# Performance work log

Hardware: AMD Instinct MI355X
Metric: run time of the kernel (lower is better)

The kernel has to match this reference:

```python
import jax, jax.numpy as jnp
import numpy as np

N_HEAD = 16


def setup_inputs() -> dict:
    key = jax.random.key(0)
    k1, k2, k3 = jax.random.split(key, 3)
    B, T, C = 2, 2048, 1024
    x = jax.random.normal(k1, (B, T, C), dtype=jnp.float32)
    Wqkv = jax.random.normal(k2, (C, 3 * C), dtype=jnp.float32) * 0.02
    bqkv = jnp.zeros((3 * C,), dtype=jnp.float32)
    Wproj = jax.random.normal(k3, (C, C), dtype=jnp.float32) * 0.02
    bproj = jnp.zeros((C,), dtype=jnp.float32)
    return {"x": x, "Wqkv": Wqkv, "bqkv": bqkv, "Wproj": Wproj, "bproj": bproj}


def reference(x, Wqkv, bqkv, Wproj, bproj):
    b, t, c = x.shape
    h = N_HEAD
    d = c // h  # head_dim
    # qkv projection, split into q,k,v per head: (b,t,3,h,d)
    qkv = (x @ Wqkv + bqkv).reshape(b, t, 3, h, d)
    q, k, v = qkv[:, :, 0], qkv[:, :, 1], qkv[:, :, 2]  # each (b,t,h,d)
    # Faithful quirk of original: n_state = head_dim // heads, scale = 1/sqrt(n_state)
    scale = jnp.float32(1.0 / np.sqrt(d // h))
    # attn_mode == 'all': dense non-causal attention
    w = jnp.einsum('bqhd,bkhd->bhqk', q, k)  # (b,h,t,t)
    w = jax.nn.softmax(w * scale, axis=-1)
    a = jnp.einsum('bhqk,bkhd->bqhd', w, v).reshape(b, t, c)
    return a @ Wproj + bproj
```

## Files before the change

### kernel.cpp

```cpp
#include <hip/hip_runtime.h>

typedef float floatx4 __attribute__((ext_vector_type(4)));
typedef float floatx16 __attribute__((ext_vector_type(16)));
typedef __bf16 bf16x8 __attribute__((ext_vector_type(8)));
typedef __bf16 bf16x4 __attribute__((ext_vector_type(4)));
typedef __bf16 bf16x2 __attribute__((ext_vector_type(2)));
typedef float floatx2 __attribute__((ext_vector_type(2)));

#define MFMA16 __builtin_amdgcn_mfma_f32_16x16x32_bf16
#define MFMA32 __builtin_amdgcn_mfma_f32_32x32x16_bf16

typedef const __attribute__((address_space(1))) void* gas_t;
typedef __attribute__((address_space(3))) void* las_t;
#define GLD16(g, l) __builtin_amdgcn_global_load_lds((gas_t)(g), (las_t)(l), 16, 0, 0)

static __device__ __forceinline__ unsigned short f2bf(float f) {
  union { float f; unsigned int u; } v; v.f = f;
  unsigned int r = v.u + 0x7fffu + ((v.u >> 16) & 1u);
  return (unsigned short)(r >> 16);
}

static __device__ __forceinline__ unsigned pk2(float a, float b) {
  floatx2 v; v[0] = a; v[1] = b;
  union { bf16x2 h; unsigned u; } u;
  u.h = __builtin_convertvector(v, bf16x2);
  return u.u;
}

static __device__ __forceinline__ void cast_transpose_tile(
    const float* __restrict__ in, unsigned short* __restrict__ out,
    int R, int C, int bx, int by) {
  const int r0 = by * 64, c0 = bx * 64;
  const int tid = threadIdx.x;
  __shared__ float tl[64][65];
  const int rr = tid >> 4, cc = (tid & 15) * 4;
#pragma unroll
  for (int i = 0; i < 4; ++i) {
    int row = rr + i * 16;
    float4 v = *(const float4*)(in + (size_t)(r0 + row) * C + c0 + cc);
    tl[row][cc] = v.x; tl[row][cc + 1] = v.y;
    tl[row][cc + 2] = v.z; tl[row][cc + 3] = v.w;
  }
  __syncthreads();
  const int cl = tid >> 2, rbase = (tid & 3) * 16;
  unsigned short o[16];
#pragma unroll
  for (int j = 0; j < 16; ++j) o[j] = f2bf(tl[rbase + j][cl]);
  unsigned short* dst = out + (size_t)(c0 + cl) * R + r0 + rbase;
  *(uint4*)dst = *(uint4*)o;
  *(uint4*)(dst + 8) = *(uint4*)(o + 8);
}

__global__ __launch_bounds__(256) void prologue_kernel(
    const float* __restrict__ x, unsigned short* __restrict__ Xb,
    const float* __restrict__ Wqkv, unsigned short* __restrict__ Wqkvt,
    const float* __restrict__ Wproj, unsigned short* __restrict__ Wprojt) {
  const int bid = blockIdx.x;
  if (bid < 4096) {
    int i = bid * 256 + threadIdx.x;
    float4 v = ((const float4*)x)[i];
    ushort4 o;
    o.x = f2bf(v.x); o.y = f2bf(v.y); o.z = f2bf(v.z); o.w = f2bf(v.w);
    ((ushort4*)Xb)[i] = o;
  } else if (bid < 4096 + 768) {
    int b2 = bid - 4096;
    cast_transpose_tile(Wqkv, Wqkvt, 1024, 3072, b2 % 48, b2 / 48);
  } else {
    int b3 = bid - 4096 - 768;
    cast_transpose_tile(Wproj, Wprojt, 1024, 1024, b3 % 16, b3 / 16);
  }
}

__global__ __launch_bounds__(256) void gemm_qkv(
    const unsigned short* __restrict__ A,
    const unsigned short* __restrict__ Bt,
    const float* __restrict__ bias,
    unsigned short* __restrict__ Q,
    unsigned short* __restrict__ Kc,
    unsigned short* __restrict__ Vt) {
  const int K = 1024;
  const int m0 = blockIdx.y * 128, n0 = blockIdx.x * 128;
  const int tid = threadIdx.x, w = tid >> 6, l = tid & 63;
  const int l16 = l & 15, lq = l >> 4;
  const int wm = w >> 1, wn = w & 1;
  const int which = n0 >> 10;

  __shared__ __align__(16) unsigned short SH[16384];
  unsigned short* As = SH;
  unsigned short* Bs = SH + 8192;

  floatx4 acc[4][4] = {};

  int sA[4], sB[4];
  unsigned ldso[4];
#pragma unroll
  for (int j = 0; j < 4; ++j) {
    int s = j * 256 + tid;
    int row = s >> 3, blk = (s & 7) ^ (row & 7);
    sA[j] = (m0 + row) * K + blk * 8;
    sB[j] = (n0 + row) * K + blk * 8;
    ldso[j] = (unsigned)(j * 256 + w * 64) * 8;
  }

  if (which == 2) {
    for (int k0 = 0; k0 < K; k0 += 64) {
      __syncthreads();
#pragma unroll
      for (int j = 0; j < 4; ++j) {
        GLD16(A + sA[j] + k0, As + ldso[j]);
        GLD16(Bt + sB[j] + k0, Bs + ldso[j]);
      }
      __syncthreads();
#pragma unroll
      for (int kk = 0; kk < 2; ++kk) {
        bf16x8 af[4], bf[4];
#pragma unroll
        for (int mi = 0; mi < 4; ++mi) {
          int row = wm * 64 + mi * 16 + l16;
          int blk = (kk * 4 + lq) ^ (l16 & 7);
          af[mi] = *(const bf16x8*)(As + row * 64 + blk * 8);
        }
#pragma unroll
        for (int ni = 0; ni < 4; ++ni) {
          int row = wn * 64 + ni * 16 + l16;
          int blk = (kk * 4 + lq) ^ (l16 & 7);
          bf[ni] = *(const bf16x8*)(Bs + row * 64 + blk * 8);
        }
#pragma unroll
        for (int ni = 0; ni < 4; ++ni)
#pragma unroll
          for (int mi = 0; mi < 4; ++mi)
            acc[mi][ni] = MFMA16(af[mi], bf[ni], acc[mi][ni], 0, 0, 0);
      }
    }
    float bv[4];
#pragma unroll
    for (int ni = 0; ni < 4; ++ni) bv[ni] = bias[n0 + wn * 64 + ni * 16 + l16];
    __syncthreads();
    unsigned short* E = SH + w * 2304;
    const int bh = (m0 >> 11) * 16 + ((n0 & 1023) >> 6) + wn;
    const int tt0 = (m0 & 2047) + wm * 64;
    const int m8 = l & 7, bc = 16 * (m8 >> 1) + 4 * (m8 & 1);
#pragma unroll
    for (int p = 0; p < 2; ++p) {
#pragma unroll
      for (int n2 = 0; n2 < 2; ++n2) {
        int ni = p * 2 + n2;
#pragma unroll
        for (int mi = 0; mi < 4; ++mi) {
          floatx4 vv = acc[mi][ni] + bv[ni];
          *(bf16x4*)(E + (n2 * 16 + l16) * 72 + mi * 16 + lq * 4) =
              __builtin_convertvector(vv, bf16x4);
        }
      }
#pragma unroll
      for (int s = 0; s < 4; ++s) {
        int dl = s * 8 + (l >> 3);
        union { bf16x4 h[2]; bf16x8 v; } uu;
        uu.h[0] = *(const bf16x4*)(E + dl * 72 + bc);
        uu.h[1] = *(const bf16x4*)(E + dl * 72 + bc + 8);
        *(bf16x8*)(Vt + ((size_t)bh * 64 + p * 32 + dl) * 2048 + tt0 +
                   m8 * 8) = uu.v;
      }
    }
  } else {
    for (int k0 = 0; k0 < K; k0 += 64) {
      __syncthreads();
#pragma unroll
      for (int j = 0; j < 4; ++j) {
        GLD16(A + sA[j] + k0, As + ldso[j]);
        GLD16(Bt + sB[j] + k0, Bs + ldso[j]);
      }
      __syncthreads();
#pragma unroll
      for (int kk = 0; kk < 2; ++kk) {
        bf16x8 af[4], bf[4];
#pragma unroll
        for (int mi = 0; mi < 4; ++mi) {
          int row = wm * 64 + mi * 16 + l16;
          int blk = (kk * 4 + lq) ^ (l16 & 7);
          af[mi] = *(const bf16x8*)(As + row * 64 + blk * 8);
        }
#pragma unroll
        for (int ni = 0; ni < 4; ++ni) {
          int row = wn * 64 + ni * 16 + l16;
          int blk = (kk * 4 + lq) ^ (l16 & 7);
          bf[ni] = *(const bf16x8*)(Bs + row * 64 + blk * 8);
        }
#pragma unroll
        for (int ni = 0; ni < 4; ++ni)
#pragma unroll
          for (int mi = 0; mi < 4; ++mi)
            acc[mi][ni] = MFMA16(bf[ni], af[mi], acc[mi][ni], 0, 0, 0);
      }
    }
    const float sc = (which == 0) ? 0.7213475204444817f : 1.0f;
    unsigned short* dst = (which == 0) ? Q : Kc;
    __syncthreads();
    unsigned short* E = SH + w * 2304;
    const int bh = (m0 >> 11) * 16 + ((n0 & 1023) >> 6) + wn;
    const size_t gbase = ((size_t)bh * 2048 + (m0 & 2047) + wm * 64) * 64;
#pragma unroll
    for (int p = 0; p < 2; ++p) {
#pragma unroll
      for (int m2 = 0; m2 < 2; ++m2) {
        int mi = p * 2 + m2;
#pragma unroll
        for (int ni = 0; ni < 4; ++ni) {
          int col0 = n0 + wn * 64 + ni * 16 + lq * 4;
          floatx4 bv = *(const floatx4*)(bias + col0);
          floatx4 vv = (acc[mi][ni] + bv) * sc;
          *(bf16x4*)(E + (m2 * 16 + l16) * 72 + ni * 16 + lq * 4) =
              __builtin_convertvector(vv, bf16x4);
        }
      }
#pragma unroll
      for (int s = 0; s < 4; ++s) {
        int rl = s * 8 + (l >> 3);
        bf16x8 vv = *(const bf16x8*)(E + rl * 72 + (l & 7) * 8);
        *(bf16x8*)(dst + gbase + (size_t)(p * 32 + rl) * 64 + (l & 7) * 8) =
            vv;
      }
    }
  }
}

__global__ __launch_bounds__(256, 2) void attn_kernel(
    const unsigned short* __restrict__ Q,
    const unsigned short* __restrict__ Kc,
    const unsigned short* __restrict__ Vt,
    unsigned short* __restrict__ AO) {
  const int T = 2048;
  const int bh = blockIdx.y, q0 = blockIdx.x * 128;
  const int tid = threadIdx.x, w = tid >> 6, l = tid & 63;
  const int r31 = l & 31, g = l >> 5;

  __shared__ __align__(16) unsigned short KVs[2][2][2][4096];

  bf16x8 qf[4];
  {
    const unsigned short* qr =
        Q + ((size_t)bh * T + q0 + w * 32 + r31) * 64 + g * 8;
#pragma unroll
    for (int ds = 0; ds < 4; ++ds) qf[ds] = *(const bf16x8*)(qr + ds * 16);
  }

  floatx16 o_acc[2] = {};
  float l_lane = 0.f;

  const unsigned short* kbase = Kc + (size_t)bh * T * 64;
  const unsigned short* vbase = Vt + (size_t)bh * 64 * T;
  int kro[2], vro[2];
  unsigned ldso[2];
#pragma unroll
  for (int j = 0; j < 2; ++j) {
    int s = j * 256 + tid;
    int row = s >> 3, blk = (s & 7) ^ (row & 7);
    kro[j] = row * 64 + blk * 8;
    vro[j] = row * T + blk * 8;
    ldso[j] = (unsigned)(j * 256 + (tid & 192)) * 8;
  }

#define STAGE_PERIOD(pp, nb)                                              \
  {                                                                       \
    _Pragma("unroll") for (int c2 = 0; c2 < 2; ++c2) {                    \
      const int c = (pp) * 2 + c2;                                        \
      _Pragma("unroll") for (int j = 0; j < 2; ++j) {                     \
        GLD16(kbase + c * 4096 + kro[j], &KVs[nb][0][c2][ldso[j]]);       \
        GLD16(vbase + c * 64 + vro[j], &KVs[nb][1][c2][ldso[j]]);         \
      }                                                                   \
    }                                                                     \
  }

  STAGE_PERIOD(0, 0);

  for (int p = 0; p < 16; ++p) {
    __syncthreads();
    if (p < 15) {
      const int nb = (p + 1) & 1;
      STAGE_PERIOD(p + 1, nb);
    }
    const int pb = p & 1;
#pragma unroll
    for (int c2 = 0; c2 < 2; ++c2) {
      const unsigned short* kb = &KVs[pb][0][c2][0];
      const unsigned short* vb = &KVs[pb][1][c2][0];

      bf16x8 pf[4];
#pragma unroll
      for (int kt = 0; kt < 2; ++kt) {
        const int row = kt * 32 + r31, rx = row & 7;
        const unsigned short* kr = kb + row * 64;
        floatx16 z = {};
#pragma unroll
        for (int ds = 0; ds < 4; ++ds)
          z = MFMA32(*(const bf16x8*)(kr + ((ds * 2 + g) ^ rx) * 8), qf[ds],
                     z, 0, 0, 0);

        float pe[16];
#pragma unroll
        for (int r = 0; r < 16; ++r) pe[r] = __builtin_amdgcn_exp2f(z[r]);
        l_lane += (((pe[0] + pe[1]) + (pe[2] + pe[3])) +
                   ((pe[4] + pe[5]) + (pe[6] + pe[7]))) +
                  (((pe[8] + pe[9]) + (pe[10] + pe[11])) +
                   ((pe[12] + pe[13]) + (pe[14] + pe[15])));
#pragma unroll
        for (int s2 = 0; s2 < 2; ++s2) {
          union { unsigned u[4]; bf16x8 v; } pu;
          pu.u[0] = pk2(pe[8 * s2 + 0], pe[8 * s2 + 1]);
          pu.u[1] = pk2(pe[8 * s2 + 2], pe[8 * s2 + 3]);
          pu.u[2] = pk2(pe[8 * s2 + 4], pe[8 * s2 + 5]);
          pu.u[3] = pk2(pe[8 * s2 + 6], pe[8 * s2 + 7]);
          pf[kt * 2 + s2] = pu.v;
        }
      }

#pragma unroll
      for (int dt = 0; dt < 2; ++dt) {
        const int row = dt * 32 + r31, rx = row & 7;
        const unsigned short* vr = vb + row * 64;
#pragma unroll
        for (int s = 0; s < 4; ++s) {
          bf16x8 vf = *(const bf16x8*)(vr + ((s * 2 + g) ^ rx) * 8);
          o_acc[dt] = MFMA32(vf, pf[s], o_acc[dt], 0, 0, 0);
        }
      }
    }
  }
#undef STAGE_PERIOD

  float ls = l_lane + __shfl_xor(l_lane, 32, 64);
  float inv = 1.0f / ls;
  const int b = bh >> 4, h = bh & 15;
  const int t = q0 + w * 32 + r31;
  unsigned short* ao = AO + ((size_t)b * 2048 + t) * 1024 + h * 64;
#pragma unroll
  for (int dt = 0; dt < 2; ++dt)
#pragma unroll
    for (int rq = 0; rq < 4; ++rq) {
      floatx4 ov;
      ov[0] = o_acc[dt][rq * 4 + 0]; ov[1] = o_acc[dt][rq * 4 + 1];
      ov[2] = o_acc[dt][rq * 4 + 2]; ov[3] = o_acc[dt][rq * 4 + 3];
      ov *= inv;
      *(bf16x4*)(ao + dt * 32 + rq * 8 + g * 4) =
          __builtin_convertvector(ov, bf16x4);
    }
}

__global__ __launch_bounds__(256) void gemm_proj(
    const unsigned short* __restrict__ A,
    const unsigned short* __restrict__ Bt,
    const float* __restrict__ bias,
    float* __restrict__ out) {
  const int K = 1024, N = 1024;
  const int m0 = blockIdx.y * 128, n0 = blockIdx.x * 64;
  const int tid = threadIdx.x, w = tid >> 6, l = tid & 63;
  const int l16 = l & 15, lq = l >> 4;

  __shared__ __align__(16) unsigned short As[128 * 64];
  __shared__ __align__(16) unsigned short Bs[64 * 64];

  floatx4 acc[2][4] = {};

  int sA[4], sB[2];
  unsigned ldsoA[4], ldsoB[2];
#pragma unroll
  for (int j = 0; j < 4; ++j) {
    int s = j * 256 + tid;
    int row = s >> 3, blk = (s & 7) ^ (row & 7);
    sA[j] = (m0 + row) * K + blk * 8;
    ldsoA[j] = (unsigned)(j * 256 + w * 64) * 8;
  }
#pragma unroll
  for (int j = 0; j < 2; ++j) {
    int s = j * 256 + tid;
    int row = s >> 3, blk = (s & 7) ^ (row & 7);
    sB[j] = (n0 + row) * K + blk * 8;
    ldsoB[j] = (unsigned)(j * 256 + w * 64) * 8;
  }

  for (int k0 = 0; k0 < K; k0 += 64) {
    __syncthreads();
#pragma unroll
    for (int j = 0; j < 4; ++j) GLD16(A + sA[j] + k0, As + ldsoA[j]);
#pragma unroll
    for (int j = 0; j < 2; ++j) GLD16(Bt + sB[j] + k0, Bs + ldsoB[j]);
    __syncthreads();
#pragma unroll
    for (int kk = 0; kk < 2; ++kk) {
      bf16x8 af[2], bf[4];
#pragma unroll
      for (int mi = 0; mi < 2; ++mi) {
        int row = w * 32 + mi * 16 + l16;
        int blk = (kk * 4 + lq) ^ (l16 & 7);
        af[mi] = *(const bf16x8*)(As + row * 64 + blk * 8);
      }
#pragma unroll
      for (int ni = 0; ni < 4; ++ni) {
        int row = ni * 16 + l16;
        int blk = (kk * 4 + lq) ^ (l16 & 7);
        bf[ni] = *(const bf16x8*)(Bs + row * 64 + blk * 8);
      }
#pragma unroll
      for (int ni = 0; ni < 4; ++ni)
#pragma unroll
        for (int mi = 0; mi < 2; ++mi)
          acc[mi][ni] = MFMA16(bf[ni], af[mi], acc[mi][ni], 0, 0, 0);
    }
  }

#pragma unroll
  for (int mi = 0; mi < 2; ++mi) {
    int t = m0 + w * 32 + mi * 16 + l16;
#pragma unroll
    for (int ni = 0; ni < 4; ++ni) {
      int col0 = n0 + ni * 16 + lq * 4;
      floatx4 bv = *(const floatx4*)(bias + col0);
      *(floatx4*)(out + (size_t)t * N + col0) = acc[mi][ni] + bv;
    }
  }
}

extern "C" void kernel_launch(void* const* d_in, const int* in_sizes, int n_in,
                              void* d_out, int out_size, void* d_ws,
                              size_t ws_size, hipStream_t stream) {
  const float* x     = (const float*)d_in[0];
  const float* Wqkv  = (const float*)d_in[1];
  const float* bqkv  = (const float*)d_in[2];
  const float* Wproj = (const float*)d_in[3];
  const float* bproj = (const float*)d_in[4];
  float* out = (float*)d_out;

  unsigned short* Xb     = (unsigned short*)d_ws;
  unsigned short* Wqkvt  = Xb + 4194304;
  unsigned short* Wprojt = Wqkvt + 3145728;
  unsigned short* Qb     = Wprojt + 1048576;
  unsigned short* Kb     = Qb + 4194304;
  unsigned short* Vtb    = Kb + 4194304;
  unsigned short* AOb    = Vtb + 4194304;

  prologue_kernel<<<5120, 256, 0, stream>>>(x, Xb, Wqkv, Wqkvt, Wproj, Wprojt);
  gemm_qkv<<<dim3(24, 32), 256, 0, stream>>>(Xb, Wqkvt, bqkv, Qb, Kb, Vtb);
  attn_kernel<<<dim3(16, 32), 256, 0, stream>>>(Qb, Kb, Vtb, AOb);
  gemm_proj<<<dim3(16, 32), 256, 0, stream>>>(AOb, Wprojt, bproj, out);
}
```

Baseline: 184.5 us.

## Double-buffer LDS tiles in QKV and projection GEMMs to overlap loads

Converts the K-loops of the QKV and output-projection GEMMs to a two-stage LDS ping-pong. The first tile is loaded before the loop, and each iteration issues the async global-to-LDS load for the next k-tile before computing on the current one. This drops one barrier per iteration and is meant to hide global load latency behind the MFMA work. In exchange, shared memory per block doubles (64 KB for the QKV GEMM), which can lower how many blocks fit on each CU.

```diff
diff --git a/kernel.cpp b/kernel.cpp
--- a/kernel.cpp
+++ b/kernel.cpp
@@ -85,9 +85,7 @@
   const int wm = w >> 1, wn = w & 1;
   const int which = n0 >> 10;
 
-  __shared__ __align__(16) unsigned short SH[16384];
-  unsigned short* As = SH;
-  unsigned short* Bs = SH + 8192;
+  __shared__ __align__(16) unsigned short SH[32768];
 
   floatx4 acc[4][4] = {};
 
@@ -102,15 +100,26 @@
     ldso[j] = (unsigned)(j * 256 + w * 64) * 8;
   }
 
+#pragma unroll
+  for (int j = 0; j < 4; ++j) {
+    GLD16(A + sA[j], SH + ldso[j]);
+    GLD16(Bt + sB[j], SH + 8192 + ldso[j]);
+  }
+
   if (which == 2) {
     for (int k0 = 0; k0 < K; k0 += 64) {
       __syncthreads();
-#pragma unroll
-      for (int j = 0; j < 4; ++j) {
-        GLD16(A + sA[j] + k0, As + ldso[j]);
-        GLD16(Bt + sB[j] + k0, Bs + ldso[j]);
-      }
-      __syncthreads();
+      const int cur = (k0 >> 6) & 1;
+      if (k0 + 64 < K) {
+        const int nxt = cur ^ 1;
+#pragma unroll
+        for (int j = 0; j < 4; ++j) {
+          GLD16(A + sA[j] + k0 + 64, SH + nxt * 16384 + ldso[j]);
+          GLD16(Bt + sB[j] + k0 + 64, SH + nxt * 16384 + 8192 + ldso[j]);
+        }
+      }
+      const unsigned short* As = SH + cur * 16384;
+      const unsigned short* Bs = SH + cur * 16384 + 8192;
 #pragma unroll
       for (int kk = 0; kk < 2; ++kk) {
         bf16x8 af[4], bf[4];
@@ -166,12 +175,17 @@
   } else {
     for (int k0 = 0; k0 < K; k0 += 64) {
       __syncthreads();
-#pragma unroll
-      for (int j = 0; j < 4; ++j) {
-        GLD16(A + sA[j] + k0, As + ldso[j]);
-        GLD16(Bt + sB[j] + k0, Bs + ldso[j]);
-      }
-      __syncthreads();
+      const int cur = (k0 >> 6) & 1;
+      if (k0 + 64 < K) {
+        const int nxt = cur ^ 1;
+#pragma unroll
+        for (int j = 0; j < 4; ++j) {
+          GLD16(A + sA[j] + k0 + 64, SH + nxt * 16384 + ldso[j]);
+          GLD16(Bt + sB[j] + k0 + 64, SH + nxt * 16384 + 8192 + ldso[j]);
+        }
+      }
+      const unsigned short* As = SH + cur * 16384;
+      const unsigned short* Bs = SH + cur * 16384 + 8192;
 #pragma unroll
       for (int kk = 0; kk < 2; ++kk) {
         bf16x8 af[4], bf[4];
@@ -357,8 +371,7 @@
   const int tid = threadIdx.x, w = tid >> 6, l = tid & 63;
   const int l16 = l & 15, lq = l >> 4;
 
-  __shared__ __align__(16) unsigned short As[128 * 64];
-  __shared__ __align__(16) unsigned short Bs[64 * 64];
+  __shared__ __align__(16) unsigned short SH[24576];
 
   floatx4 acc[2][4] = {};
 
@@ -379,13 +392,25 @@
     ldsoB[j] = (unsigned)(j * 256 + w * 64) * 8;
   }
 
+#pragma unroll
+  for (int j = 0; j < 4; ++j) GLD16(A + sA[j], SH + ldsoA[j]);
+#pragma unroll
+  for (int j = 0; j < 2; ++j) GLD16(Bt + sB[j], SH + 8192 + ldsoB[j]);
+
   for (int k0 = 0; k0 < K; k0 += 64) {
     __syncthreads();
-#pragma unroll
-    for (int j = 0; j < 4; ++j) GLD16(A + sA[j] + k0, As + ldsoA[j]);
-#pragma unroll
-    for (int j = 0; j < 2; ++j) GLD16(Bt + sB[j] + k0, Bs + ldsoB[j]);
-    __syncthreads();
+    const int cur = (k0 >> 6) & 1;
+    if (k0 + 64 < K) {
+      const int nxt = cur ^ 1;
+#pragma unroll
+      for (int j = 0; j < 4; ++j)
+        GLD16(A + sA[j] + k0 + 64, SH + nxt * 12288 + ldsoA[j]);
+#pragma unroll
+      for (int j = 0; j < 2; ++j)
+        GLD16(Bt + sB[j] + k0 + 64, SH + nxt * 12288 + 8192 + ldsoB[j]);
+    }
+    const unsigned short* As = SH + cur * 12288;
+    const unsigned short* Bs = SH + cur * 12288 + 8192;
 #pragma unroll
     for (int kk = 0; kk < 2; ++kk) {
       bf16x8 af[2], bf[4];
```

Result: faster. 164.9 us (-10.6%).
